# Optimization experiments

Measured on AMD Instinct MI355X. Metric: run time of the kernel, lower is better.

Reference implementation:

```python
import jax, jax.numpy as jnp
import numpy as np

NUM_CAPSULE = 16
DIM_CAPSULE = 64
ROUTINGS = 3
T_EPS = 1e-7


def setup_inputs() -> dict:
    key = jax.random.key(0)
    k1, k2 = jax.random.split(key)
    x = jax.random.normal(k1, (64, 512, 768), dtype=jnp.float32)
    # xavier-normal-ish init for W: [1, input_dim_capsule, num_capsule*dim_capsule]
    fan_in, fan_out = 768, NUM_CAPSULE * DIM_CAPSULE
    std = float(np.sqrt(2.0 / (fan_in + fan_out)))
    W = jax.random.normal(k2, (1, 768, NUM_CAPSULE * DIM_CAPSULE), dtype=jnp.float32) * std
    return {"x": x, "W": W}


def _squash(v, eps=T_EPS):
    # NOTE: this module's 'squash' is pure L2 normalization with eps, not the
    # classic (s^2/(1+s^2)) squash.
    s2 = jnp.sum(v * v, axis=-1, keepdims=True)
    return v / jnp.sqrt(s2 + eps)


def reference(x, W):
    B, In, _ = x.shape
    # u_hat: [B, In, num*dim] -> [B, num, In, dim]
    u = jnp.matmul(x, W).reshape(B, In, NUM_CAPSULE, DIM_CAPSULE).transpose(0, 2, 1, 3)
    b = jnp.zeros((B, NUM_CAPSULE, In), dtype=u.dtype)  # routing logits
    outputs = None
    for i in range(ROUTINGS):
        # torch code softmaxes over the num_capsule axis (after permute dance)
        c = jax.nn.softmax(b, axis=1)  # [B, num, In]
        outputs = _squash(jnp.einsum('bij,bijk->bik', c, u))  # [B, num, dim]
        if i < ROUTINGS - 1:
            b = jnp.einsum('bik,bijk->bij', outputs, u)  # [B, num, In]
    return outputs
```

## Files before the change

### kernel.cpp

```cpp
#include <hip/hip_runtime.h>
#include <hip/hip_bf16.h>
#include <stdint.h>

#define BATCH 64
#define IN_CAPS 512
#define NCAP 16
#define DCAP 64
#define GN (NCAP * DCAP)
#define GM (BATCH * IN_CAPS)
#define GK 768

typedef __bf16 bf16;
typedef __attribute__((ext_vector_type(8))) __bf16 bf16x8;
typedef __attribute__((ext_vector_type(4))) __bf16 bf16x4;
typedef __attribute__((ext_vector_type(4))) float f32x4;

__device__ inline void async16(const bf16* g, bf16* l) {
    __builtin_amdgcn_global_load_lds(
        (__attribute__((address_space(1))) void*)g,
        (__attribute__((address_space(3))) void*)l, 16, 0, 0);
}

__global__ __launch_bounds__(256) void k_convX(const float* __restrict__ X,
                                               bf16* __restrict__ Xb) {
    const size_t i = ((size_t)blockIdx.x * 256 + threadIdx.x) * 8;
    const f32x4 a = *(const f32x4*)(X + i);
    const f32x4 b = *(const f32x4*)(X + i + 4);
    bf16x8 r;
    r[0] = (bf16)a[0]; r[1] = (bf16)a[1]; r[2] = (bf16)a[2]; r[3] = (bf16)a[3];
    r[4] = (bf16)b[0]; r[5] = (bf16)b[1]; r[6] = (bf16)b[2]; r[7] = (bf16)b[3];
    *(bf16x8*)(Xb + i) = r;
}

__global__ void k_transW(const float* __restrict__ W, bf16* __restrict__ Wt) {
    __shared__ bf16 t[32][33];
    const int k0 = blockIdx.x * 32;
    const int n0 = blockIdx.y * 32;
    const int tx = threadIdx.x, ty = threadIdx.y;
#pragma unroll
    for (int r = 0; r < 4; ++r)
        t[ty + r * 8][tx] = (bf16)W[(size_t)(k0 + ty + r * 8) * GN + n0 + tx];
    __syncthreads();
#pragma unroll
    for (int r = 0; r < 4; ++r)
        Wt[(size_t)(n0 + ty + r * 8) * GK + k0 + tx] = t[tx][ty + r * 8];
}

__global__ __launch_bounds__(256) void k_gemm_async(const bf16* __restrict__ Xb,
                                                    const bf16* __restrict__ Wt,
                                                    bf16* __restrict__ U) {
    __shared__ bf16 sA[128 * 32];
    __shared__ bf16 sB[128 * 32];

    const int tid = threadIdx.x;
    const int lane = tid & 63;
    const int wave = tid >> 6;
    const int wm = wave >> 1, wn = wave & 1;
    const int m0 = blockIdx.x * 128;
    const int n0 = blockIdx.y * 128;

    const int c0 = wave * 2, c1 = wave * 2 + 1;
    const int rl = lane >> 2, cl = (lane & 3) * 8;
    const bf16* gA0 = Xb + (size_t)(m0 + c0 * 16 + rl) * GK + cl;
    const bf16* gA1 = Xb + (size_t)(m0 + c1 * 16 + rl) * GK + cl;
    const bf16* gB0 = Wt + (size_t)(n0 + c0 * 16 + rl) * GK + cl;
    const bf16* gB1 = Wt + (size_t)(n0 + c1 * 16 + rl) * GK + cl;
    bf16* lA0 = sA + c0 * 512;
    bf16* lA1 = sA + c1 * 512;
    bf16* lB0 = sB + c0 * 512;
    bf16* lB1 = sB + c1 * 512;

    f32x4 acc[4][4] = {};
    const int fr = lane & 15;
    const int fq = lane >> 4;

    for (int kt = 0; kt < GK / 32; ++kt) {
        __syncthreads();
        async16(gA0, lA0);
        async16(gA1, lA1);
        async16(gB0, lB0);
        async16(gB1, lB1);
        gA0 += 32; gA1 += 32; gB0 += 32; gB1 += 32;
        __syncthreads();

        bf16x8 af[4], bfr[4];
#pragma unroll
        for (int mi = 0; mi < 4; ++mi)
            af[mi] = *(const bf16x8*)(sA + (wm * 64 + mi * 16 + fr) * 32 + fq * 8);
#pragma unroll
        for (int ni = 0; ni < 4; ++ni)
            bfr[ni] = *(const bf16x8*)(sB + (wn * 64 + ni * 16 + fr) * 32 + fq * 8);
#pragma unroll
        for (int mi = 0; mi < 4; ++mi)
#pragma unroll
            for (int ni = 0; ni < 4; ++ni)
                acc[mi][ni] = __builtin_amdgcn_mfma_f32_16x16x32_bf16(
                    af[mi], bfr[ni], acc[mi][ni], 0, 0, 0);
    }

#pragma unroll
    for (int mi = 0; mi < 4; ++mi) {
#pragma unroll
        for (int ni = 0; ni < 4; ++ni) {
#pragma unroll
            for (int r = 0; r < 4; ++r) {
                const int m = m0 + wm * 64 + mi * 16 + fq * 4 + r;
                const int n = n0 + wn * 64 + ni * 16 + fr;
                const int bb = m >> 9, j = m & 511;
                const int ci = n >> 6, k = n & 63;
                U[(((size_t)(bb * NCAP + ci)) * IN_CAPS + j) * DCAP + k] =
                    (bf16)acc[mi][ni][r];
            }
        }
    }
}

__global__ __launch_bounds__(256) void k_gemm_inline(const float* __restrict__ X,
                                                     const bf16* __restrict__ Wt,
                                                     bf16* __restrict__ U) {
    __shared__ bf16 sA[128 * 32];
    __shared__ bf16 sB[128 * 32];
    const int tid = threadIdx.x;
    const int lane = tid & 63;
    const int wave = tid >> 6;
    const int wm = wave >> 1, wn = wave & 1;
    const int m0 = blockIdx.x * 128;
    const int n0 = blockIdx.y * 128;
    const int srow = tid >> 2;
    const int scol = (tid & 3) * 8;
    f32x4 acc[4][4] = {};
    const int fr = lane & 15;
    const int fq = lane >> 4;
    for (int kt = 0; kt < GK / 32; ++kt) {
        const int kb = kt * 32;
        bf16x8 a0, a1, b0, b1;
        {
            const float* p = X + (size_t)(m0 + srow) * GK + kb + scol;
            const f32x4 x0 = *(const f32x4*)p, x1 = *(const f32x4*)(p + 4);
            const float* q = X + (size_t)(m0 + srow + 64) * GK + kb + scol;
            const f32x4 y0 = *(const f32x4*)q, y1 = *(const f32x4*)(q + 4);
#pragma unroll
            for (int c = 0; c < 4; ++c) {
                a0[c] = (bf16)x0[c]; a0[c + 4] = (bf16)x1[c];
                a1[c] = (bf16)y0[c]; a1[c + 4] = (bf16)y1[c];
            }
        }
        b0 = *(const bf16x8*)(Wt + (size_t)(n0 + srow) * GK + kb + scol);
        b1 = *(const bf16x8*)(Wt + (size_t)(n0 + srow + 64) * GK + kb + scol);
        __syncthreads();
        *(bf16x8*)(sA + srow * 32 + scol) = a0;
        *(bf16x8*)(sA + (srow + 64) * 32 + scol) = a1;
        *(bf16x8*)(sB + srow * 32 + scol) = b0;
        *(bf16x8*)(sB + (srow + 64) * 32 + scol) = b1;
        __syncthreads();
        bf16x8 af[4], bfr[4];
#pragma unroll
        for (int mi = 0; mi < 4; ++mi)
            af[mi] = *(const bf16x8*)(sA + (wm * 64 + mi * 16 + fr) * 32 + fq * 8);
#pragma unroll
        for (int ni = 0; ni < 4; ++ni)
            bfr[ni] = *(const bf16x8*)(sB + (wn * 64 + ni * 16 + fr) * 32 + fq * 8);
#pragma unroll
        for (int mi = 0; mi < 4; ++mi)
#pragma unroll
            for (int ni = 0; ni < 4; ++ni)
                acc[mi][ni] = __builtin_amdgcn_mfma_f32_16x16x32_bf16(
                    af[mi], bfr[ni], acc[mi][ni], 0, 0, 0);
    }
#pragma unroll
    for (int mi = 0; mi < 4; ++mi) {
#pragma unroll
        for (int ni = 0; ni < 4; ++ni) {
#pragma unroll
            for (int r = 0; r < 4; ++r) {
                const int m = m0 + wm * 64 + mi * 16 + fq * 4 + r;
                const int n = n0 + wn * 64 + ni * 16 + fr;
                const int bb = m >> 9, j = m & 511;
                const int ci = n >> 6, k = n & 63;
                U[(((size_t)(bb * NCAP + ci)) * IN_CAPS + j) * DCAP + k] =
                    (bf16)acc[mi][ni][r];
            }
        }
    }
}

__global__ __launch_bounds__(256) void k_route(const bf16* __restrict__ U,
                                               float* __restrict__ BL,
                                               float* __restrict__ OutC,
                                               int mode) {
    __shared__ float sc[IN_CAPS];
    __shared__ float red[32][64];
    __shared__ float sout[64];
    const int bi = blockIdx.x;
    const int b = bi >> 4, cap = bi & 15;
    const int tid = threadIdx.x;
    const size_t ubase = (size_t)bi * IN_CAPS * DCAP;

    if (mode == 0) {
        sc[tid] = 0.0625f;
        sc[tid + 256] = 0.0625f;
    } else {
#pragma unroll
        for (int h = 0; h < 2; ++h) {
            const int j = tid + h * 256;
            const float* p = BL + (size_t)b * NCAP * IN_CAPS + j;
            float v[16], mx = -1e30f;
#pragma unroll
            for (int i = 0; i < 16; ++i) {
                v[i] = p[(size_t)i * IN_CAPS];
                mx = fmaxf(mx, v[i]);
            }
            float s = 0.f;
#pragma unroll
            for (int i = 0; i < 16; ++i) s += __expf(v[i] - mx);
            sc[j] = __expf(v[cap] - mx) / s;
        }
    }
    __syncthreads();

    const int g = tid & 7;
    const int jr = tid >> 3;

    float acc[8] = {};
#pragma unroll
    for (int it = 0; it < 16; ++it) {
        const int j = it * 32 + jr;
        const bf16x8 v = *(const bf16x8*)(U + ubase + (size_t)it * 2048 + tid * 8);
        const float cv = sc[j];
#pragma unroll
        for (int c = 0; c < 8; ++c) acc[c] += cv * (float)v[c];
    }
    *(f32x4*)(&red[jr][g * 8]) = f32x4{acc[0], acc[1], acc[2], acc[3]};
    *(f32x4*)(&red[jr][g * 8 + 4]) = f32x4{acc[4], acc[5], acc[6], acc[7]};
    __syncthreads();

    if (tid < 64) {
        float s = 0.f;
#pragma unroll
        for (int r = 0; r < 32; ++r) s += red[r][tid];
        float ss = s * s;
#pragma unroll
        for (int off = 32; off >= 1; off >>= 1) ss += __shfl_xor(ss, off);
        const float val = s * rsqrtf(ss + 1e-7f);
        sout[tid] = val;
        if (mode == 2) OutC[(size_t)bi * DCAP + tid] = val;
    }
    if (mode == 2) return;
    __syncthreads();

    const f32x4 o0 = *(const f32x4*)(sout + g * 8);
    const f32x4 o1 = *(const f32x4*)(sout + g * 8 + 4);
#pragma unroll
    for (int it = 0; it < 16; ++it) {
        const int j = it * 32 + jr;
        const bf16x8 v = *(const bf16x8*)(U + ubase + (size_t)it * 2048 + tid * 8);
        float p = o0[0] * (float)v[0] + o0[1] * (float)v[1] +
                  o0[2] * (float)v[2] + o0[3] * (float)v[3] +
                  o1[0] * (float)v[4] + o1[1] * (float)v[5] +
                  o1[2] * (float)v[6] + o1[3] * (float)v[7];
        p += __shfl_xor(p, 1);
        p += __shfl_xor(p, 2);
        p += __shfl_xor(p, 4);
        if (g == 0) BL[((size_t)b * NCAP + cap) * IN_CAPS + j] = p;
    }
}

extern "C" void kernel_launch(void* const* d_in, const int* in_sizes, int n_in,
                              void* d_out, int out_size, void* d_ws, size_t ws_size,
                              hipStream_t stream) {
    const float* X = (const float*)d_in[0];
    const float* W = (const float*)d_in[1];
    float* OutC = (float*)d_out;

    const size_t u_bytes = (size_t)BATCH * NCAP * IN_CAPS * DCAP * sizeof(bf16);
    const size_t xb_bytes = (size_t)GM * GK * sizeof(bf16);
    const size_t wt_bytes = (size_t)GN * GK * sizeof(bf16);
    const size_t bl_bytes = (size_t)BATCH * NCAP * IN_CAPS * sizeof(float);
    char* ws = (char*)d_ws;

    const size_t need_big = u_bytes + xb_bytes + wt_bytes + bl_bytes;
    const size_t need_small = u_bytes + wt_bytes + bl_bytes;

    bf16* U = (bf16*)ws;
    bf16* Wt;
    float* BL;

    if (ws_size >= need_big) {
        bf16* Xb = (bf16*)(ws + u_bytes);
        Wt = (bf16*)(ws + u_bytes + xb_bytes);
        BL = (float*)(ws + u_bytes + xb_bytes + wt_bytes);
        k_convX<<<GM * GK / (256 * 8), 256, 0, stream>>>(X, Xb);
        k_transW<<<dim3(GK / 32, GN / 32), dim3(32, 8), 0, stream>>>(W, Wt);
        k_gemm_async<<<dim3(GM / 128, GN / 128), 256, 0, stream>>>(Xb, Wt, U);
    } else if (ws_size >= need_small) {
        Wt = (bf16*)(ws + u_bytes);
        BL = (float*)(ws + u_bytes + wt_bytes);
        k_transW<<<dim3(GK / 32, GN / 32), dim3(32, 8), 0, stream>>>(W, Wt);
        k_gemm_inline<<<dim3(GM / 128, GN / 128), 256, 0, stream>>>(X, Wt, U);
    } else {
        return;
    }

    k_route<<<BATCH * NCAP, 256, 0, stream>>>(U, BL, OutC, 0);
    k_route<<<BATCH * NCAP, 256, 0, stream>>>(U, BL, OutC, 1);
    k_route<<<BATCH * NCAP, 256, 0, stream>>>(U, BL, OutC, 2);
}
```

Baseline: 277.7 us.

## Fuse routing iterations into one cooperative kernel keeping U in registers

Replaces the three per-iteration routing launches with a single cooperative kernel. Each block loads its 512x64 bf16 slice of U into registers once and reuses it across all three routing iterations, with a grid-wide sync between iterations so every block sees the other capsules' logits before its softmax. This removes two extra full reads of U from memory and two launch gaps. In exchange it needs all 1024 blocks co-resident (launch bounds of 4 blocks per CU) and pays grid-sync overhead. If the cooperative launch fails it falls back to the old three launches.

```diff
diff --git a/kernel.cpp b/kernel.cpp
--- a/kernel.cpp
+++ b/kernel.cpp
@@ -1,6 +1,9 @@
 #include <hip/hip_runtime.h>
+#include <hip/hip_cooperative_groups.h>
 #include <hip/hip_bf16.h>
 #include <stdint.h>
+
+namespace cg = cooperative_groups;
 
 #define BATCH 64
 #define IN_CAPS 512
@@ -184,6 +187,87 @@
     }
 }
 
+__global__ __launch_bounds__(256, 4) void k_route_coop(const bf16* __restrict__ U,
+                                                       float* __restrict__ BL,
+                                                       float* __restrict__ OutC) {
+    __shared__ float sc[IN_CAPS];
+    __shared__ float red[32][64];
+    __shared__ float sout[64];
+    const int bi = blockIdx.x;
+    const int b = bi >> 4, cap = bi & 15;
+    const int tid = threadIdx.x;
+    const int g = tid & 7, jr = tid >> 3;
+    const size_t ubase = (size_t)bi * IN_CAPS * DCAP;
+
+    bf16x8 v[16];
+#pragma unroll
+    for (int it = 0; it < 16; ++it)
+        v[it] = *(const bf16x8*)(U + ubase + (size_t)it * 2048 + tid * 8);
+
+    for (int iter = 0; iter < 3; ++iter) {
+        if (iter > 0) {
+#pragma unroll
+            for (int h = 0; h < 2; ++h) {
+                const int j = tid + h * 256;
+                const float* p = BL + (size_t)b * NCAP * IN_CAPS + j;
+                float vv[16], mx = -1e30f;
+#pragma unroll
+                for (int i = 0; i < 16; ++i) {
+                    vv[i] = p[(size_t)i * IN_CAPS];
+                    mx = fmaxf(mx, vv[i]);
+                }
+                float s = 0.f;
+#pragma unroll
+                for (int i = 0; i < 16; ++i) s += __expf(vv[i] - mx);
+                sc[j] = __expf(vv[cap] - mx) / s;
+            }
+            __syncthreads();
+        }
+
+        float acc[8] = {};
+#pragma unroll
+        for (int it = 0; it < 16; ++it) {
+            const float cv = (iter == 0) ? 0.0625f : sc[it * 32 + jr];
+#pragma unroll
+            for (int c = 0; c < 8; ++c) acc[c] += cv * (float)v[it][c];
+        }
+        *(f32x4*)(&red[jr][g * 8]) = f32x4{acc[0], acc[1], acc[2], acc[3]};
+        *(f32x4*)(&red[jr][g * 8 + 4]) = f32x4{acc[4], acc[5], acc[6], acc[7]};
+        __syncthreads();
+
+        if (tid < 64) {
+            float s = 0.f;
+#pragma unroll
+            for (int r = 0; r < 32; ++r) s += red[r][tid];
+            float ss = s * s;
+#pragma unroll
+            for (int off = 32; off >= 1; off >>= 1) ss += __shfl_xor(ss, off);
+            const float val = s * rsqrtf(ss + 1e-7f);
+            sout[tid] = val;
+            if (iter == 2) OutC[(size_t)bi * DCAP + tid] = val;
+        }
+        if (iter == 2) return;
+        __syncthreads();
+
+        const f32x4 o0 = *(const f32x4*)(sout + g * 8);
+        const f32x4 o1 = *(const f32x4*)(sout + g * 8 + 4);
+#pragma unroll
+        for (int it = 0; it < 16; ++it) {
+            float p = o0[0] * (float)v[it][0] + o0[1] * (float)v[it][1] +
+                      o0[2] * (float)v[it][2] + o0[3] * (float)v[it][3] +
+                      o1[0] * (float)v[it][4] + o1[1] * (float)v[it][5] +
+                      o1[2] * (float)v[it][6] + o1[3] * (float)v[it][7];
+            p += __shfl_xor(p, 1);
+            p += __shfl_xor(p, 2);
+            p += __shfl_xor(p, 4);
+            if (g == 0) BL[((size_t)b * NCAP + cap) * IN_CAPS + it * 32 + jr] = p;
+        }
+        __threadfence();
+        cg::this_grid().sync();
+        __syncthreads();
+    }
+}
+
 __global__ __launch_bounds__(256) void k_route(const bf16* __restrict__ U,
                                                float* __restrict__ BL,
                                                float* __restrict__ OutC,
@@ -301,7 +385,14 @@
         return;
     }
 
-    k_route<<<BATCH * NCAP, 256, 0, stream>>>(U, BL, OutC, 0);
-    k_route<<<BATCH * NCAP, 256, 0, stream>>>(U, BL, OutC, 1);
-    k_route<<<BATCH * NCAP, 256, 0, stream>>>(U, BL, OutC, 2);
-}
+    const bf16* Uc = U;
+    void* args[] = {(void*)&Uc, (void*)&BL, (void*)&OutC};
+    hipError_t ce = hipLaunchCooperativeKernel((void*)k_route_coop,
+                                               dim3(BATCH * NCAP), dim3(256),
+                                               args, 0, stream);
+    if (ce != hipSuccess) {
+        k_route<<<BATCH * NCAP, 256, 0, stream>>>(U, BL, OutC, 0);
+        k_route<<<BATCH * NCAP, 256, 0, stream>>>(U, BL, OutC, 1);
+        k_route<<<BATCH * NCAP, 256, 0, stream>>>(U, BL, OutC, 2);
+    }
+}
```

Measured after the change: 796.9 us. 187% more time.

## Widen routing blocks to 1024 threads and keep U tile in registers

Applied to the files above, without the earlier changes.

The routing kernel now runs 1024 threads per (batch, capsule) block. Each thread loads its 4 bf16x8 chunks of U once, up front, and keeps them in registers for both the weighted-sum pass and the agreement pass, where the old code read U twice. The reduction uses in-wave shuffles followed by a 16-row shared-memory stage, and the U loads are issued before the softmax so their latency overlaps it. The cost is larger blocks with more register pressure per thread, and a launch_bounds(1024,4) hint that may constrain the compiler.

```diff
diff --git a/kernel.cpp b/kernel.cpp
--- a/kernel.cpp
+++ b/kernel.cpp
@@ -12,7 +12,6 @@
 
 typedef __bf16 bf16;
 typedef __attribute__((ext_vector_type(8))) __bf16 bf16x8;
-typedef __attribute__((ext_vector_type(4))) __bf16 bf16x4;
 typedef __attribute__((ext_vector_type(4))) float f32x4;
 
 __device__ inline void async16(const bf16* g, bf16* l) {
@@ -184,60 +183,68 @@
     }
 }
 
-__global__ __launch_bounds__(256) void k_route(const bf16* __restrict__ U,
-                                               float* __restrict__ BL,
-                                               float* __restrict__ OutC,
-                                               int mode) {
+__global__ __launch_bounds__(1024, 4) void k_route3(const bf16* __restrict__ U,
+                                                    float* __restrict__ BL,
+                                                    float* __restrict__ OutC,
+                                                    int mode) {
     __shared__ float sc[IN_CAPS];
-    __shared__ float red[32][64];
+    __shared__ float red[16][64];
     __shared__ float sout[64];
     const int bi = blockIdx.x;
     const int b = bi >> 4, cap = bi & 15;
     const int tid = threadIdx.x;
+    const int lane = tid & 63, wave = tid >> 6;
+    const int g = tid & 7, jp = tid >> 3;
     const size_t ubase = (size_t)bi * IN_CAPS * DCAP;
 
-    if (mode == 0) {
-        sc[tid] = 0.0625f;
-        sc[tid + 256] = 0.0625f;
-    } else {
-#pragma unroll
-        for (int h = 0; h < 2; ++h) {
-            const int j = tid + h * 256;
+    bf16x8 v[4];
+#pragma unroll
+    for (int it = 0; it < 4; ++it)
+        v[it] = *(const bf16x8*)(U + ubase + (size_t)it * 8192 + tid * 8);
+
+    if (tid < IN_CAPS) {
+        if (mode == 0) {
+            sc[tid] = 0.0625f;
+        } else {
+            const int j = tid;
             const float* p = BL + (size_t)b * NCAP * IN_CAPS + j;
-            float v[16], mx = -1e30f;
+            float vv[16], mx = -1e30f;
 #pragma unroll
             for (int i = 0; i < 16; ++i) {
-                v[i] = p[(size_t)i * IN_CAPS];
-                mx = fmaxf(mx, v[i]);
+                vv[i] = p[(size_t)i * IN_CAPS];
+                mx = fmaxf(mx, vv[i]);
             }
             float s = 0.f;
 #pragma unroll
-            for (int i = 0; i < 16; ++i) s += __expf(v[i] - mx);
-            sc[j] = __expf(v[cap] - mx) / s;
+            for (int i = 0; i < 16; ++i) s += __expf(vv[i] - mx);
+            sc[j] = __expf(vv[cap] - mx) / s;
         }
     }
     __syncthreads();
 
-    const int g = tid & 7;
-    const int jr = tid >> 3;
-
     float acc[8] = {};
 #pragma unroll
-    for (int it = 0; it < 16; ++it) {
-        const int j = it * 32 + jr;
-        const bf16x8 v = *(const bf16x8*)(U + ubase + (size_t)it * 2048 + tid * 8);
-        const float cv = sc[j];
-#pragma unroll
-        for (int c = 0; c < 8; ++c) acc[c] += cv * (float)v[c];
-    }
-    *(f32x4*)(&red[jr][g * 8]) = f32x4{acc[0], acc[1], acc[2], acc[3]};
-    *(f32x4*)(&red[jr][g * 8 + 4]) = f32x4{acc[4], acc[5], acc[6], acc[7]};
+    for (int it = 0; it < 4; ++it) {
+        const float cv = sc[it * 128 + jp];
+#pragma unroll
+        for (int c = 0; c < 8; ++c) acc[c] += cv * (float)v[it][c];
+    }
+#pragma unroll
+    for (int c = 0; c < 8; ++c) {
+        acc[c] += __shfl_xor(acc[c], 8);
+        acc[c] += __shfl_xor(acc[c], 16);
+        acc[c] += __shfl_xor(acc[c], 32);
+    }
+    if (lane < 8) {
+#pragma unroll
+        for (int c = 0; c < 8; ++c) red[wave][lane * 8 + c] = acc[c];
+    }
     __syncthreads();
 
     if (tid < 64) {
         float s = 0.f;
 #pragma unroll
-        for (int r = 0; r < 32; ++r) s += red[r][tid];
+        for (int w = 0; w < 16; ++w) s += red[w][tid];
         float ss = s * s;
 #pragma unroll
         for (int off = 32; off >= 1; off >>= 1) ss += __shfl_xor(ss, off);
@@ -251,17 +258,16 @@
     const f32x4 o0 = *(const f32x4*)(sout + g * 8);
     const f32x4 o1 = *(const f32x4*)(sout + g * 8 + 4);
 #pragma unroll
-    for (int it = 0; it < 16; ++it) {
-        const int j = it * 32 + jr;
-        const bf16x8 v = *(const bf16x8*)(U + ubase + (size_t)it * 2048 + tid * 8);
-        float p = o0[0] * (float)v[0] + o0[1] * (float)v[1] +
-                  o0[2] * (float)v[2] + o0[3] * (float)v[3] +
-                  o1[0] * (float)v[4] + o1[1] * (float)v[5] +
-                  o1[2] * (float)v[6] + o1[3] * (float)v[7];
+    for (int it = 0; it < 4; ++it) {
+        float p = o0[0] * (float)v[it][0] + o0[1] * (float)v[it][1] +
+                  o0[2] * (float)v[it][2] + o0[3] * (float)v[it][3] +
+                  o1[0] * (float)v[it][4] + o1[1] * (float)v[it][5] +
+                  o1[2] * (float)v[it][6] + o1[3] * (float)v[it][7];
         p += __shfl_xor(p, 1);
         p += __shfl_xor(p, 2);
         p += __shfl_xor(p, 4);
-        if (g == 0) BL[((size_t)b * NCAP + cap) * IN_CAPS + j] = p;
+        if (g == 0)
+            BL[((size_t)b * NCAP + cap) * IN_CAPS + it * 128 + jp] = p;
     }
 }
 
@@ -301,7 +307,7 @@
         return;
     }
 
-    k_route<<<BATCH * NCAP, 256, 0, stream>>>(U, BL, OutC, 0);
-    k_route<<<BATCH * NCAP, 256, 0, stream>>>(U, BL, OutC, 1);
-    k_route<<<BATCH * NCAP, 256, 0, stream>>>(U, BL, OutC, 2);
-}
+    k_route3<<<BATCH * NCAP, 1024, 0, stream>>>(U, BL, OutC, 0);
+    k_route3<<<BATCH * NCAP, 1024, 0, stream>>>(U, BL, OutC, 1);
+    k_route3<<<BATCH * NCAP, 1024, 0, stream>>>(U, BL, OutC, 2);
+}
```

Result: slower. 285.7 us (+2.9%).
